# Optimization experiments

Hardware: AMD Instinct MI355X
Metric: run time of the kernel (lower is better)

Reference implementation:

```python
import jax, jax.numpy as jnp
import numpy as np


def _next_power2(n: int) -> int:
    return 1 << (n - 1).bit_length()


def setup_inputs() -> dict:
    key = jax.random.key(0)
    k1, k2, k3 = jax.random.split(key, 3)
    N, C, W = 32, 8, 65536
    F, WW = 16, 64
    x = jax.random.normal(k1, (N, C, W), dtype=jnp.float32)
    w = jax.random.normal(k2, (F, C, WW), dtype=jnp.float32)
    b = jax.random.normal(k3, (F,), dtype=jnp.float32)
    return {"x": x, "w": w, "b": b}


def reference(x, w, b):
    # FFT-based 1D cross-correlation (valid mode), no spectral compression
    # (preserve_energy_rate=index_back=out_size=padding=None).
    N, C, W = x.shape
    F, _, WW = w.shape
    out_W = W - WW + 1
    fftsize = _next_power2(W + WW - 1)
    Xf = jnp.fft.rfft(x, fftsize)                     # (N, C, Fr) complex
    Wf = jnp.fft.rfft(w, fftsize)                     # (F, C, Fr) complex
    # correlation = irfft(X * conj(W)); sum over channels C
    prod = jnp.einsum("ncf,kcf->nkf", Xf, jnp.conj(Wf))  # (N, F, Fr)
    out = jnp.fft.irfft(prod, fftsize)[..., :out_W]      # (N, F, out_W)
    # Original code adds bias[ff] inside the channel loop -> bias added C times.
    return out + (C * b)[None, :, None]
```

## Files before the change

### kernel.cpp

```cpp
#include <hip/hip_runtime.h>
#include <stdint.h>

typedef _Float16 half8 __attribute__((ext_vector_type(8)));
typedef _Float16 half4_t __attribute__((ext_vector_type(4)));
typedef float f32x4 __attribute__((ext_vector_type(4)));

#define N_ 32
#define C_ 8
#define W_ 65536
#define F_ 16
#define OW_ 65473
#define K_ 512
#define TILE_T 512
#define NTILES 4
#define XS 640
#define XBUF_HALFS (C_ * XS)
#define WL_HALFS (F_ * K_)

__device__ __forceinline__ uint32_t funnel16(uint32_t hi, uint32_t lo) {
  return (uint32_t)((((uint64_t)hi << 32) | (uint64_t)lo) >> 16);
}

__device__ __forceinline__ uint32_t wswz(uint32_t e ) {
  uint32_t ch = e >> 3;
  ch ^= (ch >> 6) & 7u;
  return (ch << 4) | ((e & 7u) << 1);
}

__global__ __launch_bounds__(256, 4)
void corr1d_mfma(const float* __restrict__ x, const float* __restrict__ w,
                 const float* __restrict__ b, float* __restrict__ out) {
  __shared__ __align__(16) _Float16 wl[WL_HALFS];
  __shared__ __align__(16) _Float16 xb[2][XBUF_HALFS];

  const int tid = threadIdx.x;
  const int n   = blockIdx.x >> 5;
  const int tb0 = (blockIdx.x & 31) << 11;

  const int lane = tid & 63;
  const int c15  = lane & 15;
  const int g    = lane >> 4;
  const int wv   = tid >> 6;
  const int tlw  = wv << 7;

  const float* xn = x + (size_t)n * (C_ * W_);

  #pragma unroll
  for (int j = 0; j < 8; ++j) {
    int e = (tid + 256 * j) * 4;
    f32x4 v = *reinterpret_cast<const f32x4*>(w + e);
    half4_t h; h[0] = (_Float16)v[0]; h[1] = (_Float16)v[1];
    h[2] = (_Float16)v[2]; h[3] = (_Float16)v[3];
    *reinterpret_cast<half4_t*>(reinterpret_cast<char*>(wl) + wswz((uint32_t)e)) = h;
  }

  {
    f32x4 xr[5];
    #pragma unroll
    for (int j = 0; j < 5; ++j) {
      int u = tid + 256 * j;
      int c = u / 160;
      int p = (u - c * 160) * 4;
      int gi = tb0 + p;
      if (gi < W_) xr[j] = *reinterpret_cast<const f32x4*>(xn + c * W_ + gi);
      else         xr[j] = (f32x4){0.f, 0.f, 0.f, 0.f};
    }
    #pragma unroll
    for (int j = 0; j < 5; ++j) {
      int u = tid + 256 * j;
      int c = u / 160;
      int p = (u - c * 160) * 4;
      half4_t h; h[0] = (_Float16)xr[j][0]; h[1] = (_Float16)xr[j][1];
      h[2] = (_Float16)xr[j][2]; h[3] = (_Float16)xr[j][3];
      *reinterpret_cast<half4_t*>(&xb[0][c * XS + p]) = h;
    }
  }

  const f32x4 bv4 = *reinterpret_cast<const f32x4*>(b + 4 * g);

  __syncthreads();

  int buf = 0;
  union Win { half8 h[2]; uint32_t d[8]; };

  for (int i = 0; i < NTILES; ++i) {
    const bool pf = (i + 1 < NTILES);

    f32x4 xr[5];
    if (pf) {
      const int gt0 = tb0 + (i + 1) * TILE_T;
      #pragma unroll
      for (int j = 0; j < 5; ++j) {
        int u = tid + 256 * j;
        int c = u / 160;
        int p = (u - c * 160) * 4;
        int gi = gt0 + p;
        if (gi < W_) xr[j] = *reinterpret_cast<const f32x4*>(xn + c * W_ + gi);
        else         xr[j] = (f32x4){0.f, 0.f, 0.f, 0.f};
      }
    }

    f32x4 acc[8];
    #pragma unroll
    for (int r = 0; r < 8; ++r) acc[r] = (f32x4){0.f, 0.f, 0.f, 0.f};

    const _Float16* xcur = xb[buf];
    #pragma unroll
    for (int s = 0; s < 16; ++s) {
      const uint32_t we = (uint32_t)(c15 * K_ + 32 * s + 8 * g);
      const half8 wf = *reinterpret_cast<const half8*>(
                           reinterpret_cast<const char*>(wl) + wswz(we));
      const int c  = s >> 1;
      const int jb = (s & 1) * 32;
      const int A0 = tlw + 8 * c15 + jb + 8 * g;
      Win win;
      win.h[0] = *reinterpret_cast<const half8*>(xcur + c * XS + A0);
      win.h[1] = *reinterpret_cast<const half8*>(xcur + c * XS + A0 + 8);
      #pragma unroll
      for (int r = 0; r < 8; ++r) {
        union { uint32_t d[4]; half8 h; } fr;
        const int m = r >> 1;
        if ((r & 1) == 0) {
          fr.d[0] = win.d[m];     fr.d[1] = win.d[m + 1];
          fr.d[2] = win.d[m + 2]; fr.d[3] = win.d[m + 3];
        } else {
          fr.d[0] = funnel16(win.d[m + 1], win.d[m]);
          fr.d[1] = funnel16(win.d[m + 2], win.d[m + 1]);
          fr.d[2] = funnel16(win.d[m + 3], win.d[m + 2]);
          fr.d[3] = funnel16(win.d[m + 4], win.d[m + 3]);
        }
        acc[r] = __builtin_amdgcn_mfma_f32_16x16x32_f16(wf, fr.h, acc[r], 0, 0, 0);
      }
    }

    if (pf) {
      #pragma unroll
      for (int j = 0; j < 5; ++j) {
        int u = tid + 256 * j;
        int c = u / 160;
        int p = (u - c * 160) * 4;
        half4_t h; h[0] = (_Float16)xr[j][0]; h[1] = (_Float16)xr[j][1];
        h[2] = (_Float16)xr[j][2]; h[3] = (_Float16)xr[j][3];
        *reinterpret_cast<half4_t*>(&xb[buf ^ 1][c * XS + p]) = h;
      }
    }

    __syncthreads();

    const int tl0 = tb0 + i * TILE_T + tlw + 8 * c15;
    #pragma unroll
    for (int q = 0; q < 4; ++q) {
      const int f = 4 * g + q;
      const float bias = 8.0f * bv4[q];
      f32x4 sa = { acc[0][q] + bias, acc[1][q] + bias,
                   acc[2][q] + bias, acc[3][q] + bias };
      f32x4 sb = { acc[4][q] + bias, acc[5][q] + bias,
                   acc[6][q] + bias, acc[7][q] + bias };
      float* row = out + (size_t)(n * F_ + f) * OW_ + tl0;
      if (tl0 + 8 <= OW_) {
        __builtin_memcpy(row,     &sa, 16);
        __builtin_memcpy(row + 4, &sb, 16);
      } else {
        #pragma unroll
        for (int jj = 0; jj < 8; ++jj) {
          if (tl0 + jj < OW_) row[jj] = (jj < 4) ? sa[jj] : sb[jj - 4];
        }
      }
    }

    buf ^= 1;
  }
}

extern "C" void kernel_launch(void* const* d_in, const int* in_sizes, int n_in,
                              void* d_out, int out_size, void* d_ws, size_t ws_size,
                              hipStream_t stream) {
  (void)in_sizes; (void)n_in; (void)out_size; (void)d_ws; (void)ws_size;
  const float* x = (const float*)d_in[0];
  const float* w = (const float*)d_in[1];
  const float* b = (const float*)d_in[2];
  float* out = (float*)d_out;
  corr1d_mfma<<<dim3(32 * 32), dim3(256), 0, stream>>>(x, w, b, out);
}
```

Baseline: 59.21 us.

## Give each wave a private swizzled x slice and drop block-wide barriers

Each wavefront now owns a 192-half-per-channel LDS slice and walks its own four 128-sample tiles, instead of the block sharing a double-buffered 512-sample tile. This removes the per-tile __syncthreads so waves run independently, and an XOR swizzle is added to the x slice to avoid LDS bank conflicts. The per-wave layout reloads the 64-sample halo for every wave, which adds some global reads. It relies on in-order LDS access within a wave, since the next tile overwrites the single buffer after compute. Output stores are also split into width-varied vector stores by filter row, apparently to match the alignment of rows whose length is odd.

```diff
diff --git a/kernel.cpp b/kernel.cpp
--- a/kernel.cpp
+++ b/kernel.cpp
@@ -4,6 +4,7 @@
 typedef _Float16 half8 __attribute__((ext_vector_type(8)));
 typedef _Float16 half4_t __attribute__((ext_vector_type(4)));
 typedef float f32x4 __attribute__((ext_vector_type(4)));
+typedef float f32x2 __attribute__((ext_vector_type(2)));
 
 #define N_ 32
 #define C_ 8
@@ -11,39 +12,44 @@
 #define F_ 16
 #define OW_ 65473
 #define K_ 512
-#define TILE_T 512
-#define NTILES 4
-#define XS 640
-#define XBUF_HALFS (C_ * XS)
-#define WL_HALFS (F_ * K_)
+#define XSLICE 192
+#define WL_HALFS 8192
 
 __device__ __forceinline__ uint32_t funnel16(uint32_t hi, uint32_t lo) {
   return (uint32_t)((((uint64_t)hi << 32) | (uint64_t)lo) >> 16);
 }
 
-__device__ __forceinline__ uint32_t wswz(uint32_t e ) {
+__device__ __forceinline__ uint32_t wswz(uint32_t e) {
   uint32_t ch = e >> 3;
   ch ^= (ch >> 6) & 7u;
   return (ch << 4) | ((e & 7u) << 1);
+}
+
+__device__ __forceinline__ uint32_t xswz(uint32_t byteoff) {
+  uint32_t ch = byteoff >> 4;
+  ch ^= (ch >> 3) & 7u;
+  return (byteoff & 15u) | (ch << 4);
 }
 
 __global__ __launch_bounds__(256, 4)
 void corr1d_mfma(const float* __restrict__ x, const float* __restrict__ w,
                  const float* __restrict__ b, float* __restrict__ out) {
   __shared__ __align__(16) _Float16 wl[WL_HALFS];
-  __shared__ __align__(16) _Float16 xb[2][XBUF_HALFS];
+  __shared__ __align__(16) _Float16 xsl[4][8 * XSLICE];
 
-  const int tid = threadIdx.x;
-  const int n   = blockIdx.x >> 5;
-  const int tb0 = (blockIdx.x & 31) << 11;
-
+  const int tid  = threadIdx.x;
   const int lane = tid & 63;
+  const int wv   = tid >> 6;
   const int c15  = lane & 15;
   const int g    = lane >> 4;
-  const int wv   = tid >> 6;
-  const int tlw  = wv << 7;
+  const int cc   = lane >> 3;
+  const int p0   = (lane & 7) * 24;
+
+  const int n   = blockIdx.x >> 5;
+  const int tw0 = ((blockIdx.x & 31) << 11) + (wv << 9);
 
   const float* xn = x + (size_t)n * (C_ * W_);
+  char* xwb = reinterpret_cast<char*>(xsl[wv]);
 
   #pragma unroll
   for (int j = 0; j < 8; ++j) {
@@ -55,24 +61,22 @@
   }
 
   {
-    f32x4 xr[5];
+    f32x4 xr0[6];
     #pragma unroll
-    for (int j = 0; j < 5; ++j) {
-      int u = tid + 256 * j;
-      int c = u / 160;
-      int p = (u - c * 160) * 4;
-      int gi = tb0 + p;
-      if (gi < W_) xr[j] = *reinterpret_cast<const f32x4*>(xn + c * W_ + gi);
-      else         xr[j] = (f32x4){0.f, 0.f, 0.f, 0.f};
+    for (int j = 0; j < 6; ++j) {
+      int gi = tw0 + p0 + 4 * j;
+      xr0[j] = (gi < W_) ? *reinterpret_cast<const f32x4*>(xn + cc * W_ + gi)
+                         : (f32x4){0.f, 0.f, 0.f, 0.f};
     }
+    uint32_t base = (uint32_t)(cc * XSLICE + p0) * 2u;
     #pragma unroll
-    for (int j = 0; j < 5; ++j) {
-      int u = tid + 256 * j;
-      int c = u / 160;
-      int p = (u - c * 160) * 4;
-      half4_t h; h[0] = (_Float16)xr[j][0]; h[1] = (_Float16)xr[j][1];
-      h[2] = (_Float16)xr[j][2]; h[3] = (_Float16)xr[j][3];
-      *reinterpret_cast<half4_t*>(&xb[0][c * XS + p]) = h;
+    for (int j2 = 0; j2 < 3; ++j2) {
+      half8 h;
+      h[0] = (_Float16)xr0[2*j2][0]; h[1] = (_Float16)xr0[2*j2][1];
+      h[2] = (_Float16)xr0[2*j2][2]; h[3] = (_Float16)xr0[2*j2][3];
+      h[4] = (_Float16)xr0[2*j2+1][0]; h[5] = (_Float16)xr0[2*j2+1][1];
+      h[6] = (_Float16)xr0[2*j2+1][2]; h[7] = (_Float16)xr0[2*j2+1][3];
+      *reinterpret_cast<half8*>(xwb + xswz(base + 16 * j2)) = h;
     }
   }
 
@@ -80,23 +84,17 @@
 
   __syncthreads();
 
-  int buf = 0;
   union Win { half8 h[2]; uint32_t d[8]; };
+  f32x4 xr[6];
 
-  for (int i = 0; i < NTILES; ++i) {
-    const bool pf = (i + 1 < NTILES);
-
-    f32x4 xr[5];
-    if (pf) {
-      const int gt0 = tb0 + (i + 1) * TILE_T;
+  for (int i = 0; i < 4; ++i) {
+    if (i < 3) {
+      const int t0n = tw0 + 128 * (i + 1);
       #pragma unroll
-      for (int j = 0; j < 5; ++j) {
-        int u = tid + 256 * j;
-        int c = u / 160;
-        int p = (u - c * 160) * 4;
-        int gi = gt0 + p;
-        if (gi < W_) xr[j] = *reinterpret_cast<const f32x4*>(xn + c * W_ + gi);
-        else         xr[j] = (f32x4){0.f, 0.f, 0.f, 0.f};
+      for (int j = 0; j < 6; ++j) {
+        int gi = t0n + p0 + 4 * j;
+        xr[j] = (gi < W_) ? *reinterpret_cast<const f32x4*>(xn + cc * W_ + gi)
+                          : (f32x4){0.f, 0.f, 0.f, 0.f};
       }
     }
 
@@ -104,18 +102,18 @@
     #pragma unroll
     for (int r = 0; r < 8; ++r) acc[r] = (f32x4){0.f, 0.f, 0.f, 0.f};
 
-    const _Float16* xcur = xb[buf];
     #pragma unroll
     for (int s = 0; s < 16; ++s) {
       const uint32_t we = (uint32_t)(c15 * K_ + 32 * s + 8 * g);
       const half8 wf = *reinterpret_cast<const half8*>(
                            reinterpret_cast<const char*>(wl) + wswz(we));
-      const int c  = s >> 1;
-      const int jb = (s & 1) * 32;
-      const int A0 = tlw + 8 * c15 + jb + 8 * g;
+      const int cst = s >> 1;
+      const int jb  = (s & 1) * 32;
+      const int A0  = 8 * c15 + jb + 8 * g;
+      uint32_t xb0 = (uint32_t)(cst * XSLICE + A0) * 2u;
       Win win;
-      win.h[0] = *reinterpret_cast<const half8*>(xcur + c * XS + A0);
-      win.h[1] = *reinterpret_cast<const half8*>(xcur + c * XS + A0 + 8);
+      win.h[0] = *reinterpret_cast<const half8*>(xwb + xswz(xb0));
+      win.h[1] = *reinterpret_cast<const half8*>(xwb + xswz(xb0 + 16));
       #pragma unroll
       for (int r = 0; r < 8; ++r) {
         union { uint32_t d[4]; half8 h; } fr;
@@ -133,42 +131,48 @@
       }
     }
 
-    if (pf) {
+    if (i < 3) {
+      uint32_t base = (uint32_t)(cc * XSLICE + p0) * 2u;
       #pragma unroll
-      for (int j = 0; j < 5; ++j) {
-        int u = tid + 256 * j;
-        int c = u / 160;
-        int p = (u - c * 160) * 4;
-        half4_t h; h[0] = (_Float16)xr[j][0]; h[1] = (_Float16)xr[j][1];
-        h[2] = (_Float16)xr[j][2]; h[3] = (_Float16)xr[j][3];
-        *reinterpret_cast<half4_t*>(&xb[buf ^ 1][c * XS + p]) = h;
+      for (int j2 = 0; j2 < 3; ++j2) {
+        half8 h;
+        h[0] = (_Float16)xr[2*j2][0]; h[1] = (_Float16)xr[2*j2][1];
+        h[2] = (_Float16)xr[2*j2][2]; h[3] = (_Float16)xr[2*j2][3];
+        h[4] = (_Float16)xr[2*j2+1][0]; h[5] = (_Float16)xr[2*j2+1][1];
+        h[6] = (_Float16)xr[2*j2+1][2]; h[7] = (_Float16)xr[2*j2+1][3];
+        *reinterpret_cast<half8*>(xwb + xswz(base + 16 * j2)) = h;
       }
     }
 
-    __syncthreads();
-
-    const int tl0 = tb0 + i * TILE_T + tlw + 8 * c15;
+    const int T = tw0 + 128 * i + 8 * c15;
     #pragma unroll
     for (int q = 0; q < 4; ++q) {
-      const int f = 4 * g + q;
       const float bias = 8.0f * bv4[q];
-      f32x4 sa = { acc[0][q] + bias, acc[1][q] + bias,
-                   acc[2][q] + bias, acc[3][q] + bias };
-      f32x4 sb = { acc[4][q] + bias, acc[5][q] + bias,
-                   acc[6][q] + bias, acc[7][q] + bias };
-      float* row = out + (size_t)(n * F_ + f) * OW_ + tl0;
-      if (tl0 + 8 <= OW_) {
-        __builtin_memcpy(row,     &sa, 16);
-        __builtin_memcpy(row + 4, &sb, 16);
+      float sv[8];
+      #pragma unroll
+      for (int j = 0; j < 8; ++j) sv[j] = acc[j][q] + bias;
+      float* row = out + (size_t)(n * F_ + 4 * g + q) * OW_ + T;
+      if (T + 8 <= OW_) {
+        if (q == 0) {
+          *reinterpret_cast<f32x4*>(row)     = (f32x4){sv[0], sv[1], sv[2], sv[3]};
+          *reinterpret_cast<f32x4*>(row + 4) = (f32x4){sv[4], sv[5], sv[6], sv[7]};
+        } else if (q == 2) {
+          *reinterpret_cast<f32x2*>(row)     = (f32x2){sv[0], sv[1]};
+          *reinterpret_cast<f32x2*>(row + 2) = (f32x2){sv[2], sv[3]};
+          *reinterpret_cast<f32x2*>(row + 4) = (f32x2){sv[4], sv[5]};
+          *reinterpret_cast<f32x2*>(row + 6) = (f32x2){sv[6], sv[7]};
+        } else {
+          row[0] = sv[0];
+          *reinterpret_cast<f32x2*>(row + 1) = (f32x2){sv[1], sv[2]};
+          *reinterpret_cast<f32x2*>(row + 3) = (f32x2){sv[3], sv[4]};
+          *reinterpret_cast<f32x2*>(row + 5) = (f32x2){sv[5], sv[6]};
+          row[7] = sv[7];
+        }
       } else {
         #pragma unroll
-        for (int jj = 0; jj < 8; ++jj) {
-          if (tl0 + jj < OW_) row[jj] = (jj < 4) ? sa[jj] : sb[jj - 4];
-        }
+        for (int j = 0; j < 8; ++j) if (T + j < OW_) row[j] = sv[j];
       }
     }
-
-    buf ^= 1;
   }
 }
 
```

After: 120.2 us. 103% more time.
